# Kernel optimization log

Hardware: AMD Instinct MI355X
Metric: run time of the kernel (lower is better)

## Reference

```python
import jax, jax.numpy as jnp
import numpy as np

DM = 1024        # model dim
NEXPERTS = 32    # experts per set; also group size t for the token permutation
EXPERTSETS = 4
EXPERTSIZE = 32  # dff = NEXPERTS * EXPERTSETS * EXPERTSIZE = 4096
BATCH, SEQ = 4, 2048


def setup_inputs() -> dict:
    key = jax.random.key(0)
    k0, k1, k2, k3 = jax.random.split(key, 4)
    scale = 0.02
    x = jax.random.normal(k0, (BATCH, SEQ, DM), jnp.float32)
    controller = jax.random.normal(k1, (DM, NEXPERTS, EXPERTSETS), jnp.float32) * scale
    f1 = jax.random.normal(k2, (DM, NEXPERTS, EXPERTSETS, EXPERTSIZE), jnp.float32) * scale
    bias = jnp.zeros((NEXPERTS, EXPERTSETS, EXPERTSIZE), jnp.float32)
    f2 = jax.random.normal(k3, (NEXPERTS, EXPERTSETS, EXPERTSIZE, DM), jnp.float32) * scale
    return {"x": x, "controller": controller, "f1": f1, "bias": bias, "f2": f2}


def reference(x, controller, f1, bias, f2):
    B, L, d = x.shape
    t = controller.shape[1]            # nexperts == group size
    g = L // t                         # number of token groups per example
    grouped = x.reshape(B, g, t, d)    # '... (b t) d -> ... b t d'

    # controller logits: '... t d, d e s -> ... t e s'
    logits = jnp.einsum('bgtd,des->bgtes', grouped, controller)
    # deterministic tiebreak over the token axis t (dim -3)
    tie = jnp.linspace(0.0, 1e-6, t, dtype=logits.dtype).reshape(t, 1, 1)
    logits = logits + tie
    # one-hot-ish permutation: for each (e, s) slot pick the argmax token in the group
    perm = (logits == jnp.max(logits, axis=-3, keepdims=True)).astype(x.dtype)
    perm = jax.lax.stop_gradient(perm)  # torch eq() produces detached bool mask

    # einsum 1 ('... t d, d e s f, ... t e s -> ... e s f'), done in the efficient order:
    # dispatch tokens to expert slots first, then the per-expert GEMM
    dispatched = jnp.einsum('bgtd,bgtes->bgesd', grouped, perm)
    inner = jax.nn.relu(jnp.einsum('bgesd,desf->bgesf', dispatched, f1) + bias)

    # einsum 2 + unpermute
    intermediate = jnp.einsum('bgesf,esfd->bgesd', inner, f2)
    out = jnp.einsum('bgesd,bgtes->bgtd', intermediate, perm)

    return out.reshape(B, L, d)
```

## Files before the change

kernel.cpp:

```cpp
#include <hip/hip_runtime.h>
#include <hip/hip_bf16.h>

#define NGROUP 256
#define NSLOT  128
#define TG     32
#define DM     1024
#define FF     32

#define LSCALE     4096.0f
#define INV_LSCALE (1.0f / 4096.0f)

typedef unsigned int  uint;
typedef unsigned short ushort;
typedef unsigned char uchar;
typedef __attribute__((ext_vector_type(4))) float f32x4;
typedef __attribute__((ext_vector_type(8))) short bf16x8;
typedef __attribute__((ext_vector_type(8))) _Float16 f16x8;

__device__ __forceinline__ ushort f2bf(float f) {
    uint u = __float_as_uint(f);
    u += 0x7FFFu + ((u >> 16) & 1u);
    return (ushort)(u >> 16);
}
__device__ __forceinline__ uint pk2(float a, float b) {
    return (uint)f2bf(a) | ((uint)f2bf(b) << 16);
}

__device__ __forceinline__ void gload_lds16(const void* g, void* l) {
    __builtin_amdgcn_global_load_lds(
        (const __attribute__((address_space(1))) uint*)g,
        (__attribute__((address_space(3))) uint*)l, 16, 0, 0);
}

__global__ __launch_bounds__(256) void k_fused1(
    const float* __restrict__ x, const float* __restrict__ ctrl,
    const float* __restrict__ f1, const float* __restrict__ f2,
    int* __restrict__ idx, uchar* __restrict__ idx8, ushort* __restrict__ xb,
    ushort* __restrict__ f1F, ushort* __restrict__ f2T)
{
    __shared__ float smem[4 * 32 * 64];
    const int t = threadIdx.x;

    if (blockIdx.x < 512) {
        float* Lp = smem;
        const int g  = blockIdx.x >> 1;
        const int nh = blockIdx.x & 1;
        const int w = t >> 6;
        const int lane = t & 63;
        const int lrow = lane & 15;
        const int lk8 = (lane >> 4) * 8;

        const size_t xoff0 = ((size_t)g * TG + lrow) * DM + w * 256 + lk8;
        const float* xr0 = x + xoff0;
        const float* xr1 = xr0 + 16 * DM;

        f32x4 ahh[2][4], ax[2][4];
#pragma unroll
        for (int mt = 0; mt < 2; ++mt)
#pragma unroll
            for (int nt = 0; nt < 4; ++nt) {
                ahh[mt][nt] = (f32x4){0.f, 0.f, 0.f, 0.f};
                ax[mt][nt]  = (f32x4){0.f, 0.f, 0.f, 0.f};
            }

        for (int ks = 0; ks < 8; ++ks) {
            f16x8 Ah[2], Al[2];
#pragma unroll
            for (int mt = 0; mt < 2; ++mt) {
                const float* p = (mt ? xr1 : xr0) + ks * 32;
                float xe[8];
                *(float4*)&xe[0] = *(const float4*)p;
                *(float4*)&xe[4] = *(const float4*)(p + 4);
                union { f16x8 v; _Float16 e[8]; } H, L;
#pragma unroll
                for (int j = 0; j < 8; ++j) {
                    const _Float16 h = (_Float16)xe[j];
                    H.e[j] = h;
                    L.e[j] = (_Float16)((xe[j] - (float)h) * LSCALE);
                }
                Ah[mt] = H.v; Al[mt] = L.v;
                if (nh == 0) {
                    uint4 o;
                    o.x = pk2(xe[0], xe[1]); o.y = pk2(xe[2], xe[3]);
                    o.z = pk2(xe[4], xe[5]); o.w = pk2(xe[6], xe[7]);
                    *(uint4*)(xb + xoff0 + (size_t)mt * 16 * DM + ks * 32) = o;
                }
            }
            const int kslice = w * 8 + ks;
#pragma unroll
            for (int nt = 0; nt < 4; ++nt) {
                const float* cp = ctrl
                    + (size_t)(kslice * 32 + ((lane >> 4) << 3)) * NSLOT
                    + nh * 64 + nt * 16 + (lane & 15);
                union { f16x8 v; _Float16 e[8]; } BH, BL;
#pragma unroll
                for (int j = 0; j < 8; ++j) {
                    const float c = cp[(size_t)j * NSLOT];
                    const _Float16 h = (_Float16)c;
                    BH.e[j] = h;
                    BL.e[j] = (_Float16)((c - (float)h) * LSCALE);
                }
#pragma unroll
                for (int mt = 0; mt < 2; ++mt) {
                    ahh[mt][nt] = __builtin_amdgcn_mfma_f32_16x16x32_f16(Ah[mt], BH.v, ahh[mt][nt], 0, 0, 0);
                    ax[mt][nt]  = __builtin_amdgcn_mfma_f32_16x16x32_f16(Al[mt], BH.v, ax[mt][nt], 0, 0, 0);
                    ax[mt][nt]  = __builtin_amdgcn_mfma_f32_16x16x32_f16(Ah[mt], BL.v, ax[mt][nt], 0, 0, 0);
                }
            }
        }

#pragma unroll
        for (int mt = 0; mt < 2; ++mt)
#pragma unroll
            for (int nt = 0; nt < 4; ++nt)
#pragma unroll
                for (int r = 0; r < 4; ++r) {
                    const int trow = mt * 16 + (lane >> 4) * 4 + r;
                    const int nl = nt * 16 + lrow;
                    Lp[(w * TG + trow) * 64 + nl] =
                        ahh[mt][nt][r] + ax[mt][nt][r] * INV_LSCALE;
                }
        __syncthreads();

        for (int i = t * 4; i < TG * 64; i += 256 * 4) {
            f32x4 s0 = *(const f32x4*)&Lp[i];
            f32x4 s1 = *(const f32x4*)&Lp[2048 + i];
            f32x4 s2 = *(const f32x4*)&Lp[4096 + i];
            f32x4 s3 = *(const f32x4*)&Lp[6144 + i];
            *(f32x4*)&Lp[i] = (s0 + s1) + (s2 + s3);
        }
        __syncthreads();

        if (t < 64) {
            const int n = t;
            float best = -1e30f;
            int bi = 0;
#pragma unroll
            for (int tt = 0; tt < TG; ++tt) {
                const float v = Lp[tt * 64 + n] + (float)tt * (1e-6f / 31.0f);
                if (v >= best) { best = v; bi = tt; }
            }
            idx[g * NSLOT + nh * 64 + n] = bi;
            idx8[g * NSLOT + nh * 64 + n] = (uchar)bi;
        }
    } else if (blockIdx.x < 768) {
        float* Ltr = smem;
        const int i1 = blockIdx.x - 512;
        const int es = i1 >> 1;
        const int dh = i1 & 1;
        for (int d0 = dh * 512; d0 < dh * 512 + 512; d0 += 64) {
            const int dd = t >> 2, f0 = (t & 3) * 8;
            const float* src = f1 + (size_t)(d0 + dd) * 4096 + es * FF + f0;
            float4 a = *(const float4*)src;
            float4 b = *(const float4*)(src + 4);
            __syncthreads();
            float* Lq = &Ltr[dd * 33 + f0];
            Lq[0] = a.x; Lq[1] = a.y; Lq[2] = a.z; Lq[3] = a.w;
            Lq[4] = b.x; Lq[5] = b.y; Lq[6] = b.z; Lq[7] = b.w;
            __syncthreads();
            const int f = t & 31, koct = t >> 5;
            const int nt = f >> 4;
            const int kg = d0 + koct * 8;
            const int kslice = kg >> 5;
            const int lane2 = (f & 15) | (((kg >> 3) & 3) << 4);
            uint4 o;
            o.x = pk2(Ltr[(koct * 8 + 0) * 33 + f], Ltr[(koct * 8 + 1) * 33 + f]);
            o.y = pk2(Ltr[(koct * 8 + 2) * 33 + f], Ltr[(koct * 8 + 3) * 33 + f]);
            o.z = pk2(Ltr[(koct * 8 + 4) * 33 + f], Ltr[(koct * 8 + 5) * 33 + f]);
            o.w = pk2(Ltr[(koct * 8 + 6) * 33 + f], Ltr[(koct * 8 + 7) * 33 + f]);
            *(uint4*)(f1F + ((((size_t)es * 2 + nt) * 32 + kslice) * 64 + lane2) * 8) = o;
        }
    } else {
        float* Ltr = smem;
        const int i2 = blockIdx.x - 768;
        const int es = i2 >> 2;
        const int dq = i2 & 3;
        for (int d0 = dq * 256; d0 < dq * 256 + 256; d0 += 64) {
            const int f = t >> 3, ds = (t & 7) * 8;
            const float* src = f2 + (size_t)es * (FF * DM) + f * DM + d0 + ds;
            float4 a = *(const float4*)src;
            float4 b = *(const float4*)(src + 4);
            __syncthreads();
            Ltr[(ds + 0) * 33 + f] = a.x; Ltr[(ds + 1) * 33 + f] = a.y;
            Ltr[(ds + 2) * 33 + f] = a.z; Ltr[(ds + 3) * 33 + f] = a.w;
            Ltr[(ds + 4) * 33 + f] = b.x; Ltr[(ds + 5) * 33 + f] = b.y;
            Ltr[(ds + 6) * 33 + f] = b.z; Ltr[(ds + 7) * 33 + f] = b.w;
            __syncthreads();
            const int dd = t >> 2, f0 = (t & 3) * 8;
            uint4 o;
            o.x = pk2(Ltr[dd * 33 + f0 + 0], Ltr[dd * 33 + f0 + 1]);
            o.y = pk2(Ltr[dd * 33 + f0 + 2], Ltr[dd * 33 + f0 + 3]);
            o.z = pk2(Ltr[dd * 33 + f0 + 4], Ltr[dd * 33 + f0 + 5]);
            o.w = pk2(Ltr[dd * 33 + f0 + 6], Ltr[dd * 33 + f0 + 7]);
            *(uint4*)(f2T + (size_t)es * (FF * DM) + (d0 + dd) * FF + f0) = o;
        }
    }
}

__global__ __launch_bounds__(256) void k_h_mfma(
    const ushort* __restrict__ xb, const ushort* __restrict__ f1F,
    const float* __restrict__ bias, const int* __restrict__ idx,
    ushort* __restrict__ Hb)
{
    const int es = blockIdx.x >> 2;
    const int gq = blockIdx.x & 3;
    const int w = threadIdx.x >> 6;
    const int lane = threadIdx.x & 63;
    const int lrow = lane & 15;
    const int lk8 = (lane >> 4) * 8;

    const int ga = gq * 64 + w * 16 + lrow;
    const int tok = idx[ga * NSLOT + es];
    const ushort* abase = xb + ((size_t)ga * TG + tok) * DM + lk8;
    const ushort* bbase = f1F + (size_t)es * 2 * 32 * 512 + (size_t)lane * 8;

    f32x4 acc[2] = {(f32x4){0.f, 0.f, 0.f, 0.f}, (f32x4){0.f, 0.f, 0.f, 0.f}};

#pragma unroll 4
    for (int kslice = 0; kslice < 32; ++kslice) {
        const bf16x8 A = *(const bf16x8*)(abase + kslice * 32);
#pragma unroll
        for (int nt = 0; nt < 2; ++nt) {
            const bf16x8 B = *(const bf16x8*)(bbase + ((size_t)nt * 32 + kslice) * 512);
            acc[nt] = __builtin_amdgcn_mfma_f32_16x16x32_bf16(A, B, acc[nt], 0, 0, 0);
        }
    }

#pragma unroll
    for (int nt = 0; nt < 2; ++nt) {
        const int f = nt * 16 + lrow;
        const float bv = bias[es * FF + f];
#pragma unroll
        for (int r = 0; r < 4; ++r) {
            const int g = gq * 64 + w * 16 + (lane >> 4) * 4 + r;
            const float hv = fmaxf(acc[nt][r] + bv, 0.0f);
            Hb[(size_t)g * (NSLOT * FF) + es * FF + f] = f2bf(hv);
        }
    }
}

__global__ __launch_bounds__(256) void k_out_mfma(
    const ushort* __restrict__ Hb, const ushort* __restrict__ f2T,
    const uchar* __restrict__ idx8, float* __restrict__ out)
{
    extern __shared__ char smK3[];
    float*  OL    = (float*)smK3;
    char*   Bfull = smK3 + 65536;
    char*   Aring = smK3 + 131072;

    const int G0 = (blockIdx.x >> 4) * 8;
    const int D0 = (blockIdx.x & 15) * 64;
    const int tid = threadIdx.x;
    const int w = tid >> 6;
    const int lane = tid & 63;
    const int gl = lane & 15;
    const int g8 = gl & 7;
    const int lk8 = (lane >> 4) * 8;

    for (int i = tid * 4; i < 8 * 2048; i += 1024)
        *(f32x4*)&OL[i] = (f32x4){0.f, 0.f, 0.f, 0.f};
#pragma unroll
    for (int it = 0; it < 16; ++it) {
        const int v8 = (tid + it * 256) * 8;
        const int gr = v8 >> 12;
        const int rem = v8 & 4095;
        const int s = rem >> 3;
        const uint4 q = *(const uint4*)(Hb + (size_t)(G0 + gr) * (NSLOT * FF) + rem);
        *(uint4*)(Bfull + gr * 8192 + ((s ^ gr) << 4)) = q;
    }
    uint ui[32];
    {
        const uint4* p = (const uint4*)(idx8 + (size_t)(G0 + g8) * NSLOT);
#pragma unroll
        for (int k = 0; k < 8; ++k) {
            const uint4 v = p[k];
            ui[k * 4 + 0] = v.x; ui[k * 4 + 1] = v.y;
            ui[k * 4 + 2] = v.z; ui[k * 4 + 3] = v.w;
        }
    }
    __syncthreads();

    const ushort* ap = f2T + (size_t)(D0 + w * 16 + gl) * FF + lk8;
    char* ring = Aring + w * 8192;

#pragma unroll
    for (int s = 0; s < 3; ++s) {
        gload_lds16(ap + (size_t)(2 * s)     * (FF * DM), ring + s * 2048);
        gload_lds16(ap + (size_t)(2 * s + 1) * (FF * DM), ring + s * 2048 + 1024);
    }

    float* olrow = &OL[g8 * 2048];
    const int qbase = w * 4 + (lane >> 4);
    const char* bfrow = Bfull + g8 * 8192;
    const int sq = lk8 >> 3;

#pragma unroll
    for (int c = 0; c < 64; ++c) {
        const int sl = (c + 3) & 3;
        const int e2 = ((c + 3) & 63) * 2;
        gload_lds16(ap + (size_t)e2       * (FF * DM), ring + sl * 2048);
        gload_lds16(ap + (size_t)(e2 + 1) * (FF * DM), ring + sl * 2048 + 1024);
        asm volatile("s_waitcnt vmcnt(6)" ::: "memory");

        const char* slot = ring + (c & 3) * 2048;
#pragma unroll
        for (int h = 0; h < 2; ++h) {
            const int e = c * 2 + h;
            const bf16x8 afr = *(const bf16x8*)(slot + h * 1024 + lane * 16);
            const int sB = e * 4 + sq;
            const bf16x8 bfr = *(const bf16x8*)(bfrow + ((sB ^ g8) << 4));
            const f32x4 d = __builtin_amdgcn_mfma_f32_16x16x32_bf16(
                afr, bfr, (f32x4){0.f, 0.f, 0.f, 0.f}, 0, 0, 0);
            const uint tv = (ui[e >> 2] >> ((e & 3) * 8)) & 0xFFu;
            const int q = (int)tv * 16 + qbase;
            float* olp = olrow + ((q ^ g8) << 2);
            *(f32x4*)olp = *(const f32x4*)olp + d;
        }
    }
    asm volatile("s_waitcnt vmcnt(0)" ::: "memory");
    __syncthreads();

    for (int it = 0; it < 16; ++it) {
        const int flat = tid * 4 + it * 1024;
        const int gli = flat >> 11, rem = flat & 2047;
        const int t = rem >> 6, d = rem & 63;
        const int q = rem >> 2;
        const f32x4 v = *(const f32x4*)&OL[gli * 2048 + ((q ^ gli) << 2)];
        *(f32x4*)&out[((size_t)(G0 + gli) * TG + t) * DM + D0 + d] = v;
    }
}

extern "C" void kernel_launch(void* const* d_in, const int* in_sizes, int n_in,
                              void* d_out, int out_size, void* d_ws, size_t ws_size,
                              hipStream_t stream) {
    (void)in_sizes; (void)n_in; (void)out_size; (void)ws_size;
    const float* x    = (const float*)d_in[0];
    const float* ctrl = (const float*)d_in[1];
    const float* f1   = (const float*)d_in[2];
    const float* bias = (const float*)d_in[3];
    const float* f2   = (const float*)d_in[4];
    float* out = (float*)d_out;

    char* ws = (char*)d_ws;
    int*    idx  = (int*)ws;
    ushort* Hb   = (ushort*)(ws + 131072);
    ushort* f1F  = (ushort*)(ws + 2228224);
    ushort* f2T  = (ushort*)(ws + 10616832);
    ushort* xb   = (ushort*)(ws + 19005440);
    uchar*  idx8 = (uchar*)(ws + 35782656);

    k_fused1<<<1280, 256, 0, stream>>>(x, ctrl, f1, f2, idx, idx8, xb, f1F, f2T);

    k_h_mfma<<<NSLOT * 4, 256, 0, stream>>>(xb, f1F, bias, idx, Hb);

    const size_t lds3 = 163840;
    hipFuncSetAttribute((const void*)k_out_mfma,
                        hipFuncAttributeMaxDynamicSharedMemorySize, (int)lds3);
    k_out_mfma<<<512, 256, lds3, stream>>>(Hb, f2T, idx8, out);
}
```

Baseline: 84.23 us.

## Shrink output-kernel tile to 4 groups and relayout LDS for higher occupancy

The output GEMM kernel now processes 4 token groups per block instead of 8, doubling the grid to 1024 blocks and halving LDS use (160KB to 80KB). That allows two blocks per CU. The B and output LDS buffers get a new interleaved layout that replaces the XOR swizzle. The f2 ring prefetch goes from two experts per step to one. In exchange, each f2T tile is reused across fewer groups, so global traffic for f2 roughly doubles.

```diff
diff --git a/kernel.cpp b/kernel.cpp
--- a/kernel.cpp
+++ b/kernel.cpp
@@ -244,33 +244,33 @@
     const uchar* __restrict__ idx8, float* __restrict__ out)
 {
     extern __shared__ char smK3[];
-    float*  OL    = (float*)smK3;
-    char*   Bfull = smK3 + 65536;
-    char*   Aring = smK3 + 131072;
-
-    const int G0 = (blockIdx.x >> 4) * 8;
-    const int D0 = (blockIdx.x & 15) * 64;
+    float* OL  = (float*)smK3;
+    char*  Bf  = smK3 + 32768;
+    char*  Ring = smK3 + 65536;
+
+    const int D0 = (blockIdx.x >> 6) * 64;
+    const int G0 = (blockIdx.x & 63) * 4;
     const int tid = threadIdx.x;
     const int w = tid >> 6;
     const int lane = tid & 63;
     const int gl = lane & 15;
-    const int g8 = gl & 7;
-    const int lk8 = (lane >> 4) * 8;
-
-    for (int i = tid * 4; i < 8 * 2048; i += 1024)
+    const int g4 = gl & 3;
+    const int sq = lane >> 4;
+    const int lk8 = sq * 8;
+
+    for (int i = tid * 4; i < 8192; i += 1024)
         *(f32x4*)&OL[i] = (f32x4){0.f, 0.f, 0.f, 0.f};
 #pragma unroll
-    for (int it = 0; it < 16; ++it) {
-        const int v8 = (tid + it * 256) * 8;
-        const int gr = v8 >> 12;
-        const int rem = v8 & 4095;
-        const int s = rem >> 3;
-        const uint4 q = *(const uint4*)(Hb + (size_t)(G0 + gr) * (NSLOT * FF) + rem);
-        *(uint4*)(Bfull + gr * 8192 + ((s ^ gr) << 4)) = q;
+    for (int it = 0; it < 8; ++it) {
+        const int i = tid + it * 256;
+        const int bg = i & 3, bs = (i >> 2) & 3, be = i >> 4;
+        const uint4 q = *(const uint4*)(
+            Hb + (size_t)(G0 + bg) * (NSLOT * FF) + be * FF + bs * 8);
+        *(uint4*)(Bf + i * 16) = q;
     }
     uint ui[32];
     {
-        const uint4* p = (const uint4*)(idx8 + (size_t)(G0 + g8) * NSLOT);
+        const uint4* p = (const uint4*)(idx8 + (size_t)(G0 + g4) * NSLOT);
 #pragma unroll
         for (int k = 0; k < 8; ++k) {
             const uint4 v = p[k];
@@ -281,52 +281,38 @@
     __syncthreads();
 
     const ushort* ap = f2T + (size_t)(D0 + w * 16 + gl) * FF + lk8;
-    char* ring = Aring + w * 8192;
-
-#pragma unroll
-    for (int s = 0; s < 3; ++s) {
-        gload_lds16(ap + (size_t)(2 * s)     * (FF * DM), ring + s * 2048);
-        gload_lds16(ap + (size_t)(2 * s + 1) * (FF * DM), ring + s * 2048 + 1024);
-    }
-
-    float* olrow = &OL[g8 * 2048];
-    const int qbase = w * 4 + (lane >> 4);
-    const char* bfrow = Bfull + g8 * 8192;
-    const int sq = lk8 >> 3;
-
-#pragma unroll
-    for (int c = 0; c < 64; ++c) {
-        const int sl = (c + 3) & 3;
-        const int e2 = ((c + 3) & 63) * 2;
-        gload_lds16(ap + (size_t)e2       * (FF * DM), ring + sl * 2048);
-        gload_lds16(ap + (size_t)(e2 + 1) * (FF * DM), ring + sl * 2048 + 1024);
-        asm volatile("s_waitcnt vmcnt(6)" ::: "memory");
-
-        const char* slot = ring + (c & 3) * 2048;
-#pragma unroll
-        for (int h = 0; h < 2; ++h) {
-            const int e = c * 2 + h;
-            const bf16x8 afr = *(const bf16x8*)(slot + h * 1024 + lane * 16);
-            const int sB = e * 4 + sq;
-            const bf16x8 bfr = *(const bf16x8*)(bfrow + ((sB ^ g8) << 4));
-            const f32x4 d = __builtin_amdgcn_mfma_f32_16x16x32_bf16(
-                afr, bfr, (f32x4){0.f, 0.f, 0.f, 0.f}, 0, 0, 0);
-            const uint tv = (ui[e >> 2] >> ((e & 3) * 8)) & 0xFFu;
-            const int q = (int)tv * 16 + qbase;
-            float* olp = olrow + ((q ^ g8) << 2);
-            *(f32x4*)olp = *(const f32x4*)olp + d;
-        }
+    char* ring = Ring + w * 4096;
+
+#pragma unroll
+    for (int s = 0; s < 3; ++s)
+        gload_lds16(ap + (size_t)s * (FF * DM), ring + s * 1024);
+
+    const int q4 = (w * 4 + sq) * 4 + g4;
+
+#pragma unroll
+    for (int e = 0; e < 128; ++e) {
+        gload_lds16(ap + (size_t)((e + 3) & 127) * (FF * DM),
+                    ring + ((e + 3) & 3) * 1024);
+        asm volatile("s_waitcnt vmcnt(3)" ::: "memory");
+
+        const bf16x8 afr = *(const bf16x8*)(ring + (e & 3) * 1024 + lane * 16);
+        const bf16x8 bfr = *(const bf16x8*)(Bf + ((e * 4 + sq) * 4 + g4) * 16);
+        const f32x4 d = __builtin_amdgcn_mfma_f32_16x16x32_bf16(
+            afr, bfr, (f32x4){0.f, 0.f, 0.f, 0.f}, 0, 0, 0);
+        const uint tv = (ui[e >> 2] >> ((e & 3) * 8)) & 0xFFu;
+        float* olp = &OL[tv * 256 + q4 * 4];
+        *(f32x4*)olp = *(const f32x4*)olp + d;
     }
     asm volatile("s_waitcnt vmcnt(0)" ::: "memory");
     __syncthreads();
 
-    for (int it = 0; it < 16; ++it) {
-        const int flat = tid * 4 + it * 1024;
-        const int gli = flat >> 11, rem = flat & 2047;
-        const int t = rem >> 6, d = rem & 63;
-        const int q = rem >> 2;
-        const f32x4 v = *(const f32x4*)&OL[gli * 2048 + ((q ^ gli) << 2)];
-        *(f32x4*)&out[((size_t)(G0 + gli) * TG + t) * DM + D0 + d] = v;
+#pragma unroll
+    for (int it = 0; it < 8; ++it) {
+        const int i = tid + it * 256;
+        const int t = i >> 6, rem = i & 63;
+        const int q = rem >> 2, g = rem & 3;
+        const f32x4 v = *(const f32x4*)&OL[i * 4];
+        *(f32x4*)&out[((size_t)(G0 + g) * TG + t) * DM + D0 + q * 4] = v;
     }
 }
 
@@ -353,8 +339,8 @@
 
     k_h_mfma<<<NSLOT * 4, 256, 0, stream>>>(xb, f1F, bias, idx, Hb);
 
-    const size_t lds3 = 163840;
+    const size_t lds3 = 81920;
     hipFuncSetAttribute((const void*)k_out_mfma,
                         hipFuncAttributeMaxDynamicSharedMemorySize, (int)lds3);
-    k_out_mfma<<<512, 256, lds3, stream>>>(Hb, f2T, idx8, out);
-}
+    k_out_mfma<<<16 * 64, 256, lds3, stream>>>(Hb, f2T, idx8, out);
+}
```

Measured after the change: 92.74 us. +10.1%, slower.
